# Optimization experiments

Hardware: AMD Instinct MI355X
Metric: run time of the kernel (lower is better)

The kernel has to match this reference:

```python
import jax, jax.numpy as jnp
import numpy as np

NUM_CLASSES = 100


def setup_inputs() -> dict:
    key = jax.random.key(0)
    k1, k2, k3, k4 = jax.random.split(key, 4)
    x = jax.random.normal(k1, (256, 2048), dtype=jnp.float32)
    W_model = jax.random.normal(k2, (2048, 64), dtype=jnp.float32)
    database_code = jax.random.normal(k3, (100000, 64), dtype=jnp.float32)
    database_labels = jax.random.randint(k4, (100000,), 0, NUM_CLASSES, dtype=jnp.int64)
    return {
        "x": x,
        "W_model": W_model,
        "database_code": database_code,
        "database_labels": database_labels,
        "K": 1000,
    }


def reference(x, W_model, database_code, database_labels, K):
    # model(x): single linear projection to hash-code space [B, d]
    out = x @ W_model
    # sim_score = out @ codes.T * -0.5 + num_classes/2  -> [B, N]
    sim = jnp.matmul(out, database_code.T) * -0.5 + NUM_CLASSES / 2
    # np.argpartition(sim, K)[:, :K] selects the K SMALLEST scores.
    # Equivalent set via top_k on negated scores.
    _, topk_idx = jax.lax.top_k(-sim, K)            # [B, K]
    topk_labels = database_labels[topk_idx]          # [B, K]
    # per-class histogram over the top-K retrieved labels
    classes = jnp.arange(NUM_CLASSES, dtype=topk_labels.dtype)
    counts = (topk_labels[:, :, None] == classes[None, None, :]).sum(axis=1)  # [B, C]
    probs = counts.astype(jnp.float32) / K
    return probs
```

## Files before the change

kernel.cpp:

```cpp
#include <hip/hip_runtime.h>
#include <hip/hip_fp16.h>


#define NBK 256
#define FNB 1024
#define CAPC 2048
#define BCAP 2048
#define MROWS 32
#define NCHX 64
#define NCLS 100

typedef _Float16 half8 __attribute__((ext_vector_type(8)));
typedef float floatx4 __attribute__((ext_vector_type(4)));

static __device__ __forceinline__ unsigned packh2(float a, float b) {
  _Float16 ha = (_Float16)a, hb = (_Float16)b;
  unsigned short ua, ub;
  __builtin_memcpy(&ua, &ha, 2); __builtin_memcpy(&ub, &hb, 2);
  return (unsigned)ua | ((unsigned)ub << 16);
}

static __device__ __forceinline__ void rowRange(double b1sq, double cmax,
                                                double& lo, double& inv, double& bw) {
  double hr = 0.5 * sqrt(b1sq * cmax) * 1.000001 + 9.0;
  lo = 50.0 - hr;
  bw = (2.0 * hr) / (double)NBK;
  inv = (double)NBK / (2.0 * hr);
}

static __device__ __forceinline__ void loadA(const unsigned short* __restrict__ out16,
                                             int m0, int mr, int quad,
                                             half8& a00, half8& a01, half8& a10, half8& a11) {
  const uint4* o4 = (const uint4*)out16;
  uint4 u;
  u = o4[(size_t)(m0 + mr) * 8 + quad];          __builtin_memcpy(&a00, &u, 16);
  u = o4[(size_t)(m0 + mr) * 8 + 4 + quad];      __builtin_memcpy(&a01, &u, 16);
  u = o4[(size_t)(m0 + 16 + mr) * 8 + quad];     __builtin_memcpy(&a10, &u, 16);
  u = o4[(size_t)(m0 + 16 + mr) * 8 + 4 + quad]; __builtin_memcpy(&a11, &u, 16);
}

static __device__ __forceinline__ float reduceCmax256(const float* __restrict__ slab,
                                                      int n, float* fred) {
  int tid = (int)threadIdx.x;
  float m = 0.0f;
  for (int i = tid; i < n; i += 256) m = fmaxf(m, slab[i]);
  fred[tid] = m; __syncthreads();
  for (int off = 128; off > 0; off >>= 1) {
    if (tid < off) fred[tid] = fmaxf(fred[tid], fred[tid + off]);
    __syncthreads();
  }
  float r = fred[0];
  __syncthreads();
  return r;
}

__global__ __launch_bounds__(256) void k_prep(const float* __restrict__ x,
                                              const float* __restrict__ W,
                                              const float* __restrict__ codes,
                                              const int* __restrict__ labels,
                                              int N, int Npad, int D, int B, int nCvt,
                                              unsigned short* __restrict__ codes16,
                                              float* __restrict__ cmaxSlab,
                                              double* __restrict__ out64,
                                              unsigned short* __restrict__ out16,
                                              double* __restrict__ B1sq,
                                              int* __restrict__ shiftp) {
  __shared__ double red[256];
  __shared__ float fredw[4];
  __shared__ int flag;
  int blk = (int)blockIdx.x, tid = (int)threadIdx.x;
  if (blk < nCvt) {
    int gl = tid & 15, g = tid >> 4;
    int base = blk * 256;
    float bmax = 0.0f;
#pragma unroll
    for (int p = 0; p < 16; ++p) {
      int row = base + p * 16 + g;
      float4 qv = {0.f, 0.f, 0.f, 0.f};
      if (row < N) qv = ((const float4*)(codes + (size_t)row * 64))[gl];
      uint2 o;
      o.x = packh2(qv.x, qv.y);
      o.y = packh2(qv.z, qv.w);
      ((uint2*)(codes16 + (size_t)row * 64))[gl] = o;
      double c2 = fma((double)qv.x, (double)qv.x, 0.0);
      c2 = fma((double)qv.y, (double)qv.y, c2);
      c2 = fma((double)qv.z, (double)qv.z, c2);
      c2 = fma((double)qv.w, (double)qv.w, c2);
      c2 += __shfl_xor(c2, 1, 16);
      c2 += __shfl_xor(c2, 2, 16);
      c2 += __shfl_xor(c2, 4, 16);
      c2 += __shfl_xor(c2, 8, 16);
      bmax = fmaxf(bmax, (float)(c2 * 1.000001));
    }
    int lane = tid & 63, wid = tid >> 6;
#pragma unroll
    for (int off = 32; off > 0; off >>= 1) bmax = fmaxf(bmax, __shfl_xor(bmax, off, 64));
    if (lane == 0) fredw[wid] = bmax;
    __syncthreads();
    if (tid == 0)
      cmaxSlab[blk] = fmaxf(fmaxf(fredw[0], fredw[1]), fmaxf(fredw[2], fredw[3]));
  } else if (blk < nCvt + B) {
    int b = blk - nCvt;
    int t = tid & 63, w = tid >> 6;
    int kc = D >> 2;
    int k0 = w * kc;
    const float* xr = x + (size_t)b * D;
    double a[8];
#pragma unroll
    for (int j = 0; j < 8; ++j) a[j] = 0.0;
    for (int k = k0; k < k0 + kc; k += 8) {
      float4 xv0 = *(const float4*)(xr + k);
      float4 xv1 = *(const float4*)(xr + k + 4);
      float xs[8] = {xv0.x, xv0.y, xv0.z, xv0.w, xv1.x, xv1.y, xv1.z, xv1.w};
#pragma unroll
      for (int j = 0; j < 8; ++j)
        a[j] = fma((double)xs[j], (double)W[(size_t)(k + j) * 64 + t], a[j]);
    }
    red[tid] = ((a[0] + a[1]) + (a[2] + a[3])) + ((a[4] + a[5]) + (a[6] + a[7]));
    __syncthreads();
    if (w == 0) {
      double o = 0.0;
#pragma unroll
      for (int j = 0; j < 4; ++j) o += red[t + 64 * j];
      out64[(size_t)b * 64 + t] = o;
      _Float16 h = (_Float16)(float)o;
      unsigned short us; __builtin_memcpy(&us, &h, 2);
      out16[(size_t)b * 64 + t] = us;
      red[t] = o * o;
    }
    __syncthreads();
    if (tid == 0) {
      double s = 0.0;
      for (int i = 0; i < 64; ++i) s += red[i];
      B1sq[b] = s;
    }
  } else {
    if (tid == 0) flag = 0;
    __syncthreads();
    int m = N < 256 ? N : 256;
    if (tid < m && labels[2 * tid + 1] != 0) atomicOr(&flag, 1);
    __syncthreads();
    if (tid == 0) *shiftp = flag ? 0 : 1;
  }
}

__global__ __launch_bounds__(256) void k_mhist(const unsigned short* __restrict__ codes16,
                                               const unsigned short* __restrict__ out16,
                                               const double* __restrict__ B1sq,
                                               const float* __restrict__ cmaxSlab,
                                               int nCvt, int N, int Npad, int cpb, int B,
                                               unsigned short* __restrict__ histg,
                                               unsigned char* __restrict__ buck) {
  __shared__ unsigned hist[MROWS * NBK];
  __shared__ float sP[MROWS], sQ[MROWS], fred[256];
  int tid = (int)threadIdx.x;
  int m0 = (int)blockIdx.y * MROWS, cx = (int)blockIdx.x;
  float cmax = reduceCmax256(cmaxSlab, nCvt, fred);
  for (int i = tid; i < MROWS * NBK; i += 256) hist[i] = 0u;
  if (tid < MROWS) {
    double lo, inv, bw;
    rowRange(B1sq[m0 + tid], (double)cmax, lo, inv, bw);
    sP[tid] = (float)(-0.5 * inv);
    sQ[tid] = (float)((50.0 - lo) * inv);
  }
  __syncthreads();
  int l = tid & 63, w = tid >> 6;
  int quad = l >> 4, mr = l & 15;
  half8 a00, a01, a10, a11;
  loadA(out16, m0, mr, quad, a00, a01, a10, a11);
  float P0[4], Q0[4], P1[4], Q1[4];
#pragma unroll
  for (int r = 0; r < 4; ++r) {
    P0[r] = sP[quad*4 + r];      Q0[r] = sQ[quad*4 + r];
    P1[r] = sP[16 + quad*4 + r]; Q1[r] = sQ[16 + quad*4 + r];
  }
  int cstart = cx * cpb;
  int cend = cstart + cpb; if (cend > N) cend = N;
  const uint4* c4 = (const uint4*)codes16;
  floatx4 z = {0.f, 0.f, 0.f, 0.f};
  for (int base = cstart; base < cend; base += 64) {
    int nrow = base + w * 16 + mr;
    int nc = nrow < Npad ? nrow : Npad - 1;
    uint4 ub0 = c4[(size_t)nc * 8 + quad];
    uint4 ub1 = c4[(size_t)nc * 8 + 4 + quad];
    half8 b0, b1;
    __builtin_memcpy(&b0, &ub0, 16); __builtin_memcpy(&b1, &ub1, 16);
    floatx4 d0 = __builtin_amdgcn_mfma_f32_16x16x32_f16(a00, b0, z, 0, 0, 0);
    d0 = __builtin_amdgcn_mfma_f32_16x16x32_f16(a01, b1, d0, 0, 0, 0);
    floatx4 d1 = __builtin_amdgcn_mfma_f32_16x16x32_f16(a10, b0, z, 0, 0, 0);
    d1 = __builtin_amdgcn_mfma_f32_16x16x32_f16(a11, b1, d1, 0, 0, 0);
    if (nrow < N) {
#pragma unroll
      for (int r = 0; r < 4; ++r) {
        int bk0 = (int)fmaf(d0[r], P0[r], Q0[r]);
        bk0 = bk0 < 0 ? 0 : (bk0 > NBK-1 ? NBK-1 : bk0);
        atomicAdd(&hist[(quad*4 + r) * NBK + bk0], 1u);
        buck[(size_t)(m0 + quad*4 + r) * N + nrow] = (unsigned char)bk0;
        int bk1 = (int)fmaf(d1[r], P1[r], Q1[r]);
        bk1 = bk1 < 0 ? 0 : (bk1 > NBK-1 ? NBK-1 : bk1);
        atomicAdd(&hist[(16 + quad*4 + r) * NBK + bk1], 1u);
        buck[(size_t)(m0 + 16 + quad*4 + r) * N + nrow] = (unsigned char)bk1;
      }
    }
  }
  __syncthreads();
  for (int i = tid; i < MROWS * NBK; i += 256)
    histg[((size_t)cx * B + (m0 + (i >> 8))) * NBK + (i & (NBK - 1))] =
        (unsigned short)hist[i];
}

__global__ __launch_bounds__(1024) void k_rowfinal(const float* __restrict__ codes,
                                                   const double* __restrict__ out64,
                                                   const double* __restrict__ B1sq,
                                                   const float* __restrict__ cmaxSlab,
                                                   const unsigned short* __restrict__ histg,
                                                   const unsigned char* __restrict__ buck,
                                                   const int* __restrict__ labels,
                                                   const int* __restrict__ shiftp,
                                                   const int* __restrict__ Kp,
                                                   float* __restrict__ outp,
                                                   int nCvt, int N, int B) {
  __shared__ float fredw[16];
  __shared__ unsigned sp[1024];
  __shared__ unsigned s[NBK];
  __shared__ unsigned wtot[4];
  __shared__ double key[CAPC];
  __shared__ int kidx[CAPC];
  __shared__ int blist[BCAP];
  __shared__ unsigned fhist[FNB];
  __shared__ unsigned ftot[16];
  __shared__ unsigned short tlist[CAPC];
  __shared__ double sod[64];
  __shared__ unsigned lab[NCLS];
  __shared__ unsigned ccnt, bcnt, tcnt, sCntLt;
  __shared__ int sTb, sFtb;
  int b = (int)blockIdx.x, tid = (int)threadIdx.x;
  int lane = tid & 63, wid = tid >> 6;

  {
    float m = (tid < nCvt) ? cmaxSlab[tid] : 0.0f;
    for (int i = tid + 1024; i < nCvt; i += 1024) m = fmaxf(m, cmaxSlab[i]);
#pragma unroll
    for (int off = 32; off > 0; off >>= 1) m = fmaxf(m, __shfl_xor(m, off, 64));
    if (lane == 0) fredw[wid] = m;
  }
  fhist[tid] = 0u;
  if (tid < 64) sod[tid] = out64[(size_t)b * 64 + tid];
  if (tid < NCLS) lab[tid] = 0u;
  if (tid == 0) { ccnt = 0u; bcnt = 0u; tcnt = 0u; sCntLt = 0u; sFtb = FNB; }
  __syncthreads();
  float cmax;
  { float m = fredw[0];
#pragma unroll
    for (int j = 1; j < 16; ++j) m = fmaxf(m, fredw[j]);
    cmax = m; }

  {
    int bk = tid & 255, cq = tid >> 8;
    unsigned part = 0;
#pragma unroll
    for (int t2 = 0; t2 < 16; ++t2)
      part += (unsigned)histg[((size_t)(cq * 16 + t2) * B + b) * NBK + bk];
    sp[tid] = part;
  }
  __syncthreads();
  {
    unsigned v = 0;
    if (tid < 256) {
      v = sp[tid] + sp[tid + 256] + sp[tid + 512] + sp[tid + 768];
#pragma unroll
      for (int off = 1; off < 64; off <<= 1) {
        unsigned t = (unsigned)__shfl_up((int)v, off, 64);
        if (lane >= off) v += t;
      }
      if (lane == 63) wtot[wid] = v;
    }
    __syncthreads();
    if (tid < 256) {
      for (int j = 0; j < wid; ++j) v += wtot[j];
      s[tid] = v;
    }
  }
  __syncthreads();
  unsigned K = (unsigned)Kp[0];
  if (tid < 256) {
    unsigned prev = tid ? s[tid - 1] : 0u;
    if (s[tid] >= K && prev < K) sTb = tid;
  }
  __syncthreads();
  int tb = sTb;
  double lo, inv, bwd;
  rowRange(B1sq[b], (double)cmax, lo, inv, bwd);
  double S = sqrt(B1sq[b] * (double)cmax);
  double Mtot = 2.0 * (0.5 * S * 1.1e-3 + 0.05) + 1e-3;
  int q = (int)ceil(Mtot / bwd);
  int belowMax = tb - 1 - q;
  int candMax = tb + 1 + q;
  if (candMax > NBK - 1) candMax = NBK - 1;
  unsigned btot = (belowMax >= 0) ? s[belowMax] : 0u;
  int shift = *shiftp;

  {
    const uint4* bw16 = (const uint4*)(buck + (size_t)b * N);
    int nw16 = N >> 4;
#define CLS1(nn, bkv)                                                  \
    { int bk_ = (int)(bkv);                                            \
      if (bk_ <= belowMax) {                                           \
        unsigned p_ = atomicAdd(&bcnt, 1u);                            \
        if (p_ < BCAP) blist[p_] = (nn);                               \
      } else if (bk_ <= candMax) {                                     \
        unsigned p_ = atomicAdd(&ccnt, 1u);                            \
        if (p_ < CAPC) kidx[p_] = (nn);                                \
      } }
#define PROCV(vv, nb)                                                  \
    { unsigned w_;                                                     \
      w_ = (vv).x; CLS1((nb)+0,  w_ & 0xFF) CLS1((nb)+1,  (w_>>8)&0xFF)\
                   CLS1((nb)+2,  (w_>>16)&0xFF) CLS1((nb)+3,  w_>>24)  \
      w_ = (vv).y; CLS1((nb)+4,  w_ & 0xFF) CLS1((nb)+5,  (w_>>8)&0xFF)\
                   CLS1((nb)+6,  (w_>>16)&0xFF) CLS1((nb)+7,  w_>>24)  \
      w_ = (vv).z; CLS1((nb)+8,  w_ & 0xFF) CLS1((nb)+9,  (w_>>8)&0xFF)\
                   CLS1((nb)+10, (w_>>16)&0xFF) CLS1((nb)+11, w_>>24)  \
      w_ = (vv).w; CLS1((nb)+12, w_ & 0xFF) CLS1((nb)+13, (w_>>8)&0xFF)\
                   CLS1((nb)+14, (w_>>16)&0xFF) CLS1((nb)+15, w_>>24) }
    for (int i = tid; i < nw16; i += 2048) {
      uint4 v0 = bw16[i];
      int i1 = i + 1024; bool h1 = i1 < nw16;
      uint4 v1 = {0u, 0u, 0u, 0u};
      if (h1) v1 = bw16[i1];
      PROCV(v0, i << 4)
      if (h1) PROCV(v1, i1 << 4)
    }
#undef PROCV
    for (int n = (nw16 << 4) + tid; n < N; n += 1024) {
      CLS1(n, buck[(size_t)b * N + n])
    }
#undef CLS1
  }
  __syncthreads();

  {
    int bm = (int)bcnt; if (bm > BCAP) bm = BCAP;
    for (int i = tid; i < bm; i += 1024)
      atomicAdd(&lab[labels[(size_t)blist[i] << shift]], 1u);
  }
  int cc = (int)ccnt; if (cc > CAPC) cc = CAPC;
  {
    int g = tid >> 4, gl = tid & 15;
    for (int i = g; i < cc; i += 64) {
      int n = kidx[i];
      float4 qv = ((const float4*)(codes + (size_t)n * 64))[gl];
      double p = fma((double)qv.x, sod[gl*4+0], 0.0);
      p = fma((double)qv.y, sod[gl*4+1], p);
      p = fma((double)qv.z, sod[gl*4+2], p);
      p = fma((double)qv.w, sod[gl*4+3], p);
      p += __shfl_xor(p, 1, 16);
      p += __shfl_xor(p, 2, 16);
      p += __shfl_xor(p, 4, 16);
      p += __shfl_xor(p, 8, 16);
      if (gl == 0) key[i] = fma(p, -0.5, 50.0);
    }
  }
  __syncthreads();

  int need = (int)K - (int)btot;
  double fLo = lo + (double)(belowMax + 1) * bwd - Mtot;
  double fInv = (double)FNB / ((double)(candMax - belowMax) * bwd + 2.0 * Mtot);
  for (int i = tid; i < cc; i += 1024) {
    int fb = (int)((key[i] - fLo) * fInv);
    fb = fb < 0 ? 0 : (fb > FNB - 1 ? FNB - 1 : fb);
    atomicAdd(&fhist[fb], 1u);
  }
  __syncthreads();
  {
    unsigned v = fhist[tid];
#pragma unroll
    for (int off = 1; off < 64; off <<= 1) {
      unsigned t = (unsigned)__shfl_up((int)v, off, 64);
      if (lane >= off) v += t;
    }
    if (lane == 63) ftot[wid] = v;
    sp[tid] = v;
  }
  __syncthreads();
  {
    unsigned off = 0;
    for (int j = 0; j < wid; ++j) off += ftot[j];
    unsigned ci = sp[tid] + off;
    unsigned ce = ci - fhist[tid];
    if ((int)ci >= need && (int)ce < need) { sFtb = tid; sCntLt = ce; }
  }
  __syncthreads();
  int ftb = sFtb;
  for (int i = tid; i < cc; i += 1024) {
    int fb = (int)((key[i] - fLo) * fInv);
    fb = fb < 0 ? 0 : (fb > FNB - 1 ? FNB - 1 : fb);
    if (fb < ftb) {
      atomicAdd(&lab[labels[(size_t)kidx[i] << shift]], 1u);
    } else if (fb == ftb) {
      unsigned p_ = atomicAdd(&tcnt, 1u);
      if (p_ < CAPC) tlist[p_] = (unsigned short)i;
    }
  }
  __syncthreads();
  {
    int tn = (int)tcnt; if (tn > CAPC) tn = CAPC;
    int rem = need - (int)sCntLt;
    for (int j = tid; j < tn; j += 1024) {
      int i = (int)tlist[j];
      double ki = key[i]; int ii = kidx[i];
      int rank = 0;
      for (int j2 = 0; j2 < tn; ++j2) {
        int i2 = (int)tlist[j2];
        double k2 = key[i2];
        rank += (k2 < ki || (k2 == ki && kidx[i2] < ii)) ? 1 : 0;
      }
      if (rank < rem) atomicAdd(&lab[labels[(size_t)ii << shift]], 1u);
    }
  }
  __syncthreads();
  double Kd = (double)K;
  for (int c = tid; c < NCLS; c += 1024)
    outp[b * NCLS + c] = (float)((double)lab[c] / Kd);
}

extern "C" void kernel_launch(void* const* d_in, const int* in_sizes, int n_in,
                              void* d_out, int out_size, void* d_ws, size_t ws_size,
                              hipStream_t stream) {
  const float* x     = (const float*)d_in[0];
  const float* W     = (const float*)d_in[1];
  const float* codes = (const float*)d_in[2];
  const int* labels  = (const int*)d_in[3];
  const int* Kp      = (const int*)d_in[4];

  const int B = out_size / NCLS;
  const int N = in_sizes[3];
  const int D = in_sizes[0] / B;
  const int Npad = (N + 255) & ~255;
  const int cpb = (((N + NCHX - 1) / NCHX) + 63) & ~63;
  const int nCvt = Npad / 256;

  char* p = (char*)d_ws;
  double* out64      = (double*)p;   p += (size_t)B * 64 * sizeof(double);
  unsigned short* out16 = (unsigned short*)p; p += (size_t)B * 64 * 2;
  double* B1sq       = (double*)p;   p += (size_t)B * sizeof(double);
  int* shiftp        = (int*)p;      p += 64;
  float* cmaxSlab    = (float*)p;    p += 4096;
  unsigned short* histg = (unsigned short*)p; p += (size_t)NCHX * B * NBK * 2;
  unsigned char* buck   = (unsigned char*)p;  p += (size_t)B * N;
  unsigned short* codes16 = (unsigned short*)p;

  k_prep<<<nCvt + B + 1, 256, 0, stream>>>(x, W, codes, labels, N, Npad, D, B, nCvt,
                                           codes16, cmaxSlab, out64, out16, B1sq, shiftp);
  k_mhist<<<dim3(NCHX, B / MROWS), 256, 0, stream>>>(codes16, out16, B1sq, cmaxSlab,
                                                     nCvt, N, Npad, cpb, B, histg, buck);
  k_rowfinal<<<B, 1024, 0, stream>>>(codes, out64, B1sq, cmaxSlab, histg, buck,
                                     labels, shiftp, Kp, (float*)d_out, nCvt, N, B);
}
```

Measured before the change: 160.4 us.

## Widen prep kernel to 1024 threads with shared-memory x staging

The prep kernel now runs 1024-thread blocks. Code-conversion blocks handle four rows per thread instead of looping over sixteen, and the projection blocks split the K dimension across 16 waves after staging the x row in shared memory. The final squared-norm reduction uses wave shuffles instead of a serial single-thread loop. This aims to cut per-block latency in the prep stage, at the cost of heavier LDS use (about 16KB plus 8KB) and possible lower occupancy. The shared xs buffer is fixed at 2048 floats, which assumes D<=2048.

```diff
diff --git a/kernel.cpp b/kernel.cpp
--- a/kernel.cpp
+++ b/kernel.cpp
@@ -54,85 +54,94 @@
   return r;
 }
 
-__global__ __launch_bounds__(256) void k_prep(const float* __restrict__ x,
-                                              const float* __restrict__ W,
-                                              const float* __restrict__ codes,
-                                              const int* __restrict__ labels,
-                                              int N, int Npad, int D, int B, int nCvt,
-                                              unsigned short* __restrict__ codes16,
-                                              float* __restrict__ cmaxSlab,
-                                              double* __restrict__ out64,
-                                              unsigned short* __restrict__ out16,
-                                              double* __restrict__ B1sq,
-                                              int* __restrict__ shiftp) {
-  __shared__ double red[256];
-  __shared__ float fredw[4];
+__global__ __launch_bounds__(1024) void k_prep(const float* __restrict__ x,
+                                               const float* __restrict__ W,
+                                               const float* __restrict__ codes,
+                                               const int* __restrict__ labels,
+                                               int N, int Npad, int D, int B, int nCvt,
+                                               unsigned short* __restrict__ codes16,
+                                               float* __restrict__ cmaxSlab,
+                                               double* __restrict__ out64,
+                                               unsigned short* __restrict__ out16,
+                                               double* __restrict__ B1sq,
+                                               int* __restrict__ shiftp) {
+  __shared__ double red[1024];
+  __shared__ float xs[2048];
+  __shared__ float fredw[16];
   __shared__ int flag;
   int blk = (int)blockIdx.x, tid = (int)threadIdx.x;
+  int lane = tid & 63, wid = tid >> 6;
   if (blk < nCvt) {
     int gl = tid & 15, g = tid >> 4;
     int base = blk * 256;
+    int r0 = base + g, r1 = base + 64 + g, r2 = base + 128 + g, r3 = base + 192 + g;
+    float4 q0 = {0.f,0.f,0.f,0.f}, q1 = q0, q2 = q0, q3 = q0;
+    if (r0 < N) q0 = ((const float4*)(codes + (size_t)r0 * 64))[gl];
+    if (r1 < N) q1 = ((const float4*)(codes + (size_t)r1 * 64))[gl];
+    if (r2 < N) q2 = ((const float4*)(codes + (size_t)r2 * 64))[gl];
+    if (r3 < N) q3 = ((const float4*)(codes + (size_t)r3 * 64))[gl];
+    uint2 o0, o1, o2, o3;
+    o0.x = packh2(q0.x, q0.y); o0.y = packh2(q0.z, q0.w);
+    o1.x = packh2(q1.x, q1.y); o1.y = packh2(q1.z, q1.w);
+    o2.x = packh2(q2.x, q2.y); o2.y = packh2(q2.z, q2.w);
+    o3.x = packh2(q3.x, q3.y); o3.y = packh2(q3.z, q3.w);
+    ((uint2*)(codes16 + (size_t)r0 * 64))[gl] = o0;
+    ((uint2*)(codes16 + (size_t)r1 * 64))[gl] = o1;
+    ((uint2*)(codes16 + (size_t)r2 * 64))[gl] = o2;
+    ((uint2*)(codes16 + (size_t)r3 * 64))[gl] = o3;
     float bmax = 0.0f;
-#pragma unroll
-    for (int p = 0; p < 16; ++p) {
-      int row = base + p * 16 + g;
-      float4 qv = {0.f, 0.f, 0.f, 0.f};
-      if (row < N) qv = ((const float4*)(codes + (size_t)row * 64))[gl];
-      uint2 o;
-      o.x = packh2(qv.x, qv.y);
-      o.y = packh2(qv.z, qv.w);
-      ((uint2*)(codes16 + (size_t)row * 64))[gl] = o;
-      double c2 = fma((double)qv.x, (double)qv.x, 0.0);
-      c2 = fma((double)qv.y, (double)qv.y, c2);
-      c2 = fma((double)qv.z, (double)qv.z, c2);
-      c2 = fma((double)qv.w, (double)qv.w, c2);
-      c2 += __shfl_xor(c2, 1, 16);
-      c2 += __shfl_xor(c2, 2, 16);
-      c2 += __shfl_xor(c2, 4, 16);
-      c2 += __shfl_xor(c2, 8, 16);
-      bmax = fmaxf(bmax, (float)(c2 * 1.000001));
-    }
-    int lane = tid & 63, wid = tid >> 6;
+#define NRM(qv)                                                            \
+    { double c2 = fma((double)(qv).x, (double)(qv).x, 0.0);                \
+      c2 = fma((double)(qv).y, (double)(qv).y, c2);                        \
+      c2 = fma((double)(qv).z, (double)(qv).z, c2);                        \
+      c2 = fma((double)(qv).w, (double)(qv).w, c2);                        \
+      c2 += __shfl_xor(c2, 1, 16); c2 += __shfl_xor(c2, 2, 16);            \
+      c2 += __shfl_xor(c2, 4, 16); c2 += __shfl_xor(c2, 8, 16);            \
+      bmax = fmaxf(bmax, (float)(c2 * 1.000001)); }
+    NRM(q0) NRM(q1) NRM(q2) NRM(q3)
+#undef NRM
 #pragma unroll
     for (int off = 32; off > 0; off >>= 1) bmax = fmaxf(bmax, __shfl_xor(bmax, off, 64));
     if (lane == 0) fredw[wid] = bmax;
     __syncthreads();
-    if (tid == 0)
-      cmaxSlab[blk] = fmaxf(fmaxf(fredw[0], fredw[1]), fmaxf(fredw[2], fredw[3]));
+    if (tid == 0) {
+      float m = fredw[0];
+#pragma unroll
+      for (int j = 1; j < 16; ++j) m = fmaxf(m, fredw[j]);
+      cmaxSlab[blk] = m;
+    }
   } else if (blk < nCvt + B) {
     int b = blk - nCvt;
+    const float* xr = x + (size_t)b * D;
+    for (int i = tid; i < (D >> 1); i += 1024)
+      ((float2*)xs)[i] = ((const float2*)xr)[i];
+    __syncthreads();
     int t = tid & 63, w = tid >> 6;
-    int kc = D >> 2;
+    int kc = D >> 4;
     int k0 = w * kc;
-    const float* xr = x + (size_t)b * D;
     double a[8];
 #pragma unroll
     for (int j = 0; j < 8; ++j) a[j] = 0.0;
+#pragma unroll 2
     for (int k = k0; k < k0 + kc; k += 8) {
-      float4 xv0 = *(const float4*)(xr + k);
-      float4 xv1 = *(const float4*)(xr + k + 4);
-      float xs[8] = {xv0.x, xv0.y, xv0.z, xv0.w, xv1.x, xv1.y, xv1.z, xv1.w};
 #pragma unroll
       for (int j = 0; j < 8; ++j)
-        a[j] = fma((double)xs[j], (double)W[(size_t)(k + j) * 64 + t], a[j]);
+        a[j] = fma((double)xs[k + j], (double)W[(size_t)(k + j) * 64 + t], a[j]);
     }
     red[tid] = ((a[0] + a[1]) + (a[2] + a[3])) + ((a[4] + a[5]) + (a[6] + a[7]));
     __syncthreads();
     if (w == 0) {
       double o = 0.0;
 #pragma unroll
-      for (int j = 0; j < 4; ++j) o += red[t + 64 * j];
+      for (int j = 0; j < 16; ++j) o += red[t + 64 * j];
       out64[(size_t)b * 64 + t] = o;
       _Float16 h = (_Float16)(float)o;
       unsigned short us; __builtin_memcpy(&us, &h, 2);
       out16[(size_t)b * 64 + t] = us;
-      red[t] = o * o;
-    }
-    __syncthreads();
-    if (tid == 0) {
-      double s = 0.0;
-      for (int i = 0; i < 64; ++i) s += red[i];
-      B1sq[b] = s;
+      double sq = o * o;
+#pragma unroll
+      for (int off = 1; off < 64; off <<= 1) sq += __shfl_xor(sq, off, 64);
+      if (t == 0) B1sq[b] = sq;
     }
   } else {
     if (tid == 0) flag = 0;
@@ -449,8 +458,8 @@
   unsigned char* buck   = (unsigned char*)p;  p += (size_t)B * N;
   unsigned short* codes16 = (unsigned short*)p;
 
-  k_prep<<<nCvt + B + 1, 256, 0, stream>>>(x, W, codes, labels, N, Npad, D, B, nCvt,
-                                           codes16, cmaxSlab, out64, out16, B1sq, shiftp);
+  k_prep<<<nCvt + B + 1, 1024, 0, stream>>>(x, W, codes, labels, N, Npad, D, B, nCvt,
+                                            codes16, cmaxSlab, out64, out16, B1sq, shiftp);
   k_mhist<<<dim3(NCHX, B / MROWS), 256, 0, stream>>>(codes16, out16, B1sq, cmaxSlab,
                                                      nCvt, N, Npad, cpb, B, histg, buck);
   k_rowfinal<<<B, 1024, 0, stream>>>(codes, out64, B1sq, cmaxSlab, histg, buck,
```

Result: faster. 152.4 us (-5.0%).
